# Optimization experiments

Hardware: AMD Instinct MI355X
Metric: run time of the kernel (lower is better)

The kernel has to match this reference:

```python
import jax, jax.numpy as jnp
import numpy as np

N = 500_000   # points
D = 256       # num_features
K = 512       # number of foreground instances
OUT = 32      # out_channels


def setup_inputs() -> dict:
    key = jax.random.key(0)
    k1, k2, k3, k4, k5, k6 = jax.random.split(key, 6)
    features = jax.random.normal(k1, (N, D), dtype=jnp.float32)
    coords = jax.random.normal(k2, (N, 3), dtype=jnp.float32)
    # ids in [-1, K), -1 = background (guaranteed present in expectation)
    instance_ids = jax.random.randint(k3, (N,), -1, K, dtype=jnp.int32)
    # MLP params (torch Linear weight [out,in] stored transposed as [in,out])
    W1 = jax.random.normal(k4, (D, 64), dtype=jnp.float32) * (1.0 / np.sqrt(D))
    W2 = jax.random.normal(k5, (64, 64), dtype=jnp.float32) * (1.0 / np.sqrt(64))
    W3 = jax.random.normal(k6, (64, OUT), dtype=jnp.float32) * (1.0 / np.sqrt(64))
    b3 = jnp.zeros((OUT,), dtype=jnp.float32)
    return {
        "features": features,
        "coords": coords,
        "instance_ids": instance_ids,
        "num_instances": K,
        "W1": W1,
        "W2": W2,
        "W3": W3,
        "b3": b3,
    }


def reference(features, coords, instance_ids, num_instances, W1, W2, W3, b3):
    # Background (-1) points are routed to an extra dummy segment and dropped.
    seg = jnp.where(instance_ids >= 0, instance_ids, num_instances)
    nseg = num_instances + 1

    ones = jnp.ones((features.shape[0],), dtype=features.dtype)
    counts = jax.ops.segment_sum(ones, seg, num_segments=nseg)[:num_instances]  # [K]
    denom = jnp.maximum(counts, 1.0)[:, None]

    feat_sum = jax.ops.segment_sum(features, seg, num_segments=nseg)[:num_instances]  # [K, D]
    embeddings = feat_sum / denom  # per-instance feature mean (== prototype.F.mean(0))

    coord_sum = jax.ops.segment_sum(coords, seg, num_segments=nseg)[:num_instances]  # [K, 3]
    centroids = coord_sum / denom  # scatter_mean of coordinates

    # tiny MLP: Linear(D,64,no bias) -> ReLU -> Linear(64,64,no bias) -> ReLU -> Linear(64,OUT,bias)
    h = jax.nn.relu(embeddings @ W1)
    h = jax.nn.relu(h @ W2)
    out = h @ W3 + b3  # [K, OUT]

    return embeddings, centroids, out
```

## Files before the change

### kernel.cpp

```cpp
#include <hip/hip_runtime.h>

#define DFEAT 256
#define KINST 512
#define OUTC  32
#define CHUNK 4096
#define BUCKET_CHUNK 2048

__global__ __launch_bounds__(256) void hist_kernel(const int* __restrict__ ids,
                                                   int* __restrict__ counts, int n) {
    __shared__ int hist[KINST];
    int start = blockIdx.x * CHUNK;
    int len = n - start;
    if (len > CHUNK) len = CHUNK;
    for (int b = threadIdx.x; b < KINST; b += 256) hist[b] = 0;
    __syncthreads();
    for (int l = threadIdx.x; l < len; l += 256) {
        int id = ids[start + l];
        if (id >= 0) atomicAdd(&hist[id], 1);
    }
    __syncthreads();
    for (int b = threadIdx.x; b < KINST; b += 256) {
        int c = hist[b];
        if (c) atomicAdd(&counts[b], c);
    }
}

__global__ void scan_kernel(const int* __restrict__ counts, int* __restrict__ offsets) {
    __shared__ int s[KINST];
    int t = threadIdx.x;
    int c = counts[t];
    s[t] = c;
    __syncthreads();
    for (int off = 1; off < KINST; off <<= 1) {
        int add = (t >= off) ? s[t - off] : 0;
        __syncthreads();
        s[t] += add;
        __syncthreads();
    }
    offsets[t] = s[t] - c;
}

__global__ __launch_bounds__(256) void scatter2_kernel(const int* __restrict__ ids,
                                                       const int* __restrict__ offsets,
                                                       int* __restrict__ cursor,
                                                       int* __restrict__ bucket, int n) {
    __shared__ int ids_s[CHUNK];
    __shared__ int hist[KINST];
    __shared__ int bases[KINST];
    __shared__ int lcur[KINST];
    int start = blockIdx.x * CHUNK;
    int len = n - start;
    if (len > CHUNK) len = CHUNK;
    for (int b = threadIdx.x; b < KINST; b += 256) { hist[b] = 0; lcur[b] = 0; }
    for (int l = threadIdx.x; l < len; l += 256) ids_s[l] = ids[start + l];
    __syncthreads();
    for (int l = threadIdx.x; l < len; l += 256) {
        int id = ids_s[l];
        if (id >= 0) atomicAdd(&hist[id], 1);
    }
    __syncthreads();
    for (int b = threadIdx.x; b < KINST; b += 256) {
        int c = hist[b];
        bases[b] = c ? (offsets[b] + atomicAdd(&cursor[b], c)) : 0;
    }
    __syncthreads();
    for (int l = threadIdx.x; l < len; l += 256) {
        int id = ids_s[l];
        if (id >= 0) {
            int w = atomicAdd(&lcur[id], 1);
            bucket[bases[id] + w] = start + l;
        }
    }
}

__global__ __launch_bounds__(512) void gather_kernel(const float4* __restrict__ feat4,
                                                     const float* __restrict__ coords,
                                                     const int* __restrict__ bucket,
                                                     const int* __restrict__ offsets,
                                                     const int* __restrict__ counts,
                                                     float* __restrict__ emb_out,
                                                     float* __restrict__ cent_out) {
    __shared__ int bl[BUCKET_CHUNK];
    __shared__ float red[2048];

    int k   = blockIdx.x;
    int off = offsets[k];
    int cnt = counts[k];

    int sub = threadIdx.x >> 6;
    int f4  = threadIdx.x & 63;

    float a0x = 0.f, a0y = 0.f, a0z = 0.f, a0w = 0.f;
    float a1x = 0.f, a1y = 0.f, a1z = 0.f, a1w = 0.f;
    float cx = 0.f, cy = 0.f, cz = 0.f;

    for (int base = 0; base < cnt; base += BUCKET_CHUNK) {
        int chunk = cnt - base;
        if (chunk > BUCKET_CHUNK) chunk = BUCKET_CHUNK;
        for (int t = threadIdx.x; t < chunk; t += 512) bl[t] = bucket[off + base + t];
        __syncthreads();

        for (int t = threadIdx.x; t < chunk; t += 512) {
            long r = bl[t];
            cx += coords[r * 3 + 0];
            cy += coords[r * 3 + 1];
            cz += coords[r * 3 + 2];
        }

        int i = sub;
        for (; i + 8 < chunk; i += 16) {
            int r0 = bl[i];
            int r1 = bl[i + 8];
            float4 v0 = feat4[(long)r0 * 64 + f4];
            float4 v1 = feat4[(long)r1 * 64 + f4];
            a0x += v0.x; a0y += v0.y; a0z += v0.z; a0w += v0.w;
            a1x += v1.x; a1y += v1.y; a1z += v1.z; a1w += v1.w;
        }
        if (i < chunk) {
            int r = bl[i];
            float4 v = feat4[(long)r * 64 + f4];
            a0x += v.x; a0y += v.y; a0z += v.z; a0w += v.w;
        }
        __syncthreads();
    }

    a0x += a1x; a0y += a1y; a0z += a1z; a0w += a1w;

    float inv = 1.0f / (float)(cnt > 1 ? cnt : 1);

    red[threadIdx.x * 4 + 0] = a0x;
    red[threadIdx.x * 4 + 1] = a0y;
    red[threadIdx.x * 4 + 2] = a0z;
    red[threadIdx.x * 4 + 3] = a0w;
    __syncthreads();
    if (sub == 0) {
        float tx = 0.f, ty = 0.f, tz = 0.f, tw = 0.f;
        #pragma unroll
        for (int s = 0; s < 8; s++) {
            int b = (s * 64 + f4) * 4;
            tx += red[b + 0]; ty += red[b + 1]; tz += red[b + 2]; tw += red[b + 3];
        }
        float4 o;
        o.x = tx * inv; o.y = ty * inv; o.z = tz * inv; o.w = tw * inv;
        ((float4*)emb_out)[(long)k * 64 + f4] = o;
    }
    __syncthreads();

    red[threadIdx.x]        = cx;
    red[512  + threadIdx.x] = cy;
    red[1024 + threadIdx.x] = cz;
    __syncthreads();
    for (int s = 256; s > 0; s >>= 1) {
        if (threadIdx.x < s) {
            red[threadIdx.x]        += red[threadIdx.x + s];
            red[512  + threadIdx.x] += red[512  + threadIdx.x + s];
            red[1024 + threadIdx.x] += red[1024 + threadIdx.x + s];
        }
        __syncthreads();
    }
    if (threadIdx.x == 0) {
        cent_out[k * 3 + 0] = red[0]    * inv;
        cent_out[k * 3 + 1] = red[512]  * inv;
        cent_out[k * 3 + 2] = red[1024] * inv;
    }
}

__global__ __launch_bounds__(64) void mlp_kernel(const float* __restrict__ emb,
                                                 const float* __restrict__ W1,
                                                 const float* __restrict__ W2,
                                                 const float* __restrict__ W3,
                                                 const float* __restrict__ b3,
                                                 float* __restrict__ mlp_out) {
    int k = blockIdx.x;
    int j = threadIdx.x;
    __shared__ float e[DFEAT];
    __shared__ float h1[64];
    __shared__ float h2[64];

    float4 ev = ((const float4*)emb)[(long)k * 64 + j];
    e[j * 4 + 0] = ev.x; e[j * 4 + 1] = ev.y; e[j * 4 + 2] = ev.z; e[j * 4 + 3] = ev.w;
    __syncthreads();

    float acc = 0.f;
    #pragma unroll 8
    for (int d = 0; d < DFEAT; d++) acc += e[d] * W1[d * 64 + j];
    h1[j] = fmaxf(acc, 0.f);
    __syncthreads();

    acc = 0.f;
    #pragma unroll 8
    for (int d = 0; d < 64; d++) acc += h1[d] * W2[d * 64 + j];
    h2[j] = fmaxf(acc, 0.f);
    __syncthreads();

    if (j < OUTC) {
        float o = b3[j];
        #pragma unroll 8
        for (int d = 0; d < 64; d++) o += h2[d] * W3[d * OUTC + j];
        mlp_out[k * OUTC + j] = o;
    }
}

extern "C" void kernel_launch(void* const* d_in, const int* in_sizes, int n_in,
                              void* d_out, int out_size, void* d_ws, size_t ws_size,
                              hipStream_t stream) {
    const float* features = (const float*)d_in[0];
    const float* coords   = (const float*)d_in[1];
    const int*   ids      = (const int*)d_in[2];
    const float* W1 = (const float*)d_in[4];
    const float* W2 = (const float*)d_in[5];
    const float* W3 = (const float*)d_in[6];
    const float* b3 = (const float*)d_in[7];

    int n = in_sizes[2];

    float* out      = (float*)d_out;
    float* emb_out  = out;
    float* cent_out = out + (long)KINST * DFEAT;
    float* mlp_out  = cent_out + (long)KINST * 3;

    char* ws = (char*)d_ws;
    int* counts  = (int*)(ws + 0);
    int* cursor  = (int*)(ws + 2048);
    int* offsets = (int*)(ws + 4096);
    int* bucket  = (int*)(ws + 6144);

    hipMemsetAsync(d_ws, 0, 4096, stream);

    int blocksHS = (n + CHUNK - 1) / CHUNK;
    hist_kernel<<<blocksHS, 256, 0, stream>>>(ids, counts, n);
    scan_kernel<<<1, KINST, 0, stream>>>(counts, offsets);
    scatter2_kernel<<<blocksHS, 256, 0, stream>>>(ids, offsets, cursor, bucket, n);
    gather_kernel<<<KINST, 512, 0, stream>>>((const float4*)features, coords, bucket,
                                             offsets, counts, emb_out, cent_out);
    mlp_kernel<<<KINST, 64, 0, stream>>>(emb_out, W1, W2, W3, b3, mlp_out);
}
```

Before: 711.9 us.

## Fuse centroid sums into histogram, precompute per-block bases, fuse MLP into gather

```diff
diff --git a/kernel.cpp b/kernel.cpp
--- a/kernel.cpp
+++ b/kernel.cpp
@@ -6,26 +6,51 @@
 #define CHUNK 4096
 #define BUCKET_CHUNK 2048
 
-__global__ __launch_bounds__(256) void hist_kernel(const int* __restrict__ ids,
-                                                   int* __restrict__ counts, int n) {
+__global__ __launch_bounds__(256) void hist_coords_kernel(
+        const int* __restrict__ ids, const float* __restrict__ coords,
+        int* __restrict__ counts, float* __restrict__ csum,
+        int* __restrict__ blockhist, int n) {
     __shared__ int hist[KINST];
+    __shared__ float sx[KINST], sy[KINST], sz[KINST];
     int start = blockIdx.x * CHUNK;
     int len = n - start;
     if (len > CHUNK) len = CHUNK;
-    for (int b = threadIdx.x; b < KINST; b += 256) hist[b] = 0;
+    for (int b = threadIdx.x; b < KINST; b += 256) {
+        hist[b] = 0; sx[b] = 0.f; sy[b] = 0.f; sz[b] = 0.f;
+    }
     __syncthreads();
     for (int l = threadIdx.x; l < len; l += 256) {
         int id = ids[start + l];
-        if (id >= 0) atomicAdd(&hist[id], 1);
+        if (id >= 0) {
+            long p = (long)(start + l) * 3;
+            float x = coords[p + 0];
+            float y = coords[p + 1];
+            float z = coords[p + 2];
+            atomicAdd(&hist[id], 1);
+            atomicAdd(&sx[id], x);
+            atomicAdd(&sy[id], y);
+            atomicAdd(&sz[id], z);
+        }
     }
     __syncthreads();
     for (int b = threadIdx.x; b < KINST; b += 256) {
         int c = hist[b];
-        if (c) atomicAdd(&counts[b], c);
-    }
-}
-
-__global__ void scan_kernel(const int* __restrict__ counts, int* __restrict__ offsets) {
+        blockhist[blockIdx.x * KINST + b] = c;
+        if (c) {
+            atomicAdd(&counts[b], c);
+            atomicAdd(&csum[b * 3 + 0], sx[b]);
+            atomicAdd(&csum[b * 3 + 1], sy[b]);
+            atomicAdd(&csum[b * 3 + 2], sz[b]);
+        }
+    }
+}
+
+__global__ void scan_kernel(const int* __restrict__ counts,
+                            const float* __restrict__ csum,
+                            int* __restrict__ offsets,
+                            const int* __restrict__ blockhist,
+                            int* __restrict__ blockbase,
+                            float* __restrict__ cent_out, int nblk) {
     __shared__ int s[KINST];
     int t = threadIdx.x;
     int c = counts[t];
@@ -37,35 +62,36 @@
         s[t] += add;
         __syncthreads();
     }
-    offsets[t] = s[t] - c;
-}
-
-__global__ __launch_bounds__(256) void scatter2_kernel(const int* __restrict__ ids,
-                                                       const int* __restrict__ offsets,
-                                                       int* __restrict__ cursor,
-                                                       int* __restrict__ bucket, int n) {
-    __shared__ int ids_s[CHUNK];
-    __shared__ int hist[KINST];
+    int excl = s[t] - c;
+    offsets[t] = excl;
+
+    float inv = 1.0f / (float)(c > 1 ? c : 1);
+    cent_out[t * 3 + 0] = csum[t * 3 + 0] * inv;
+    cent_out[t * 3 + 1] = csum[t * 3 + 1] * inv;
+    cent_out[t * 3 + 2] = csum[t * 3 + 2] * inv;
+
+    int base = excl;
+    for (int blk = 0; blk < nblk; ++blk) {
+        blockbase[blk * KINST + t] = base;
+        base += blockhist[blk * KINST + t];
+    }
+}
+
+__global__ __launch_bounds__(256) void scatter_kernel(
+        const int* __restrict__ ids, const int* __restrict__ blockbase,
+        int* __restrict__ bucket, int n) {
     __shared__ int bases[KINST];
     __shared__ int lcur[KINST];
     int start = blockIdx.x * CHUNK;
     int len = n - start;
     if (len > CHUNK) len = CHUNK;
-    for (int b = threadIdx.x; b < KINST; b += 256) { hist[b] = 0; lcur[b] = 0; }
-    for (int l = threadIdx.x; l < len; l += 256) ids_s[l] = ids[start + l];
+    for (int b = threadIdx.x; b < KINST; b += 256) {
+        bases[b] = blockbase[blockIdx.x * KINST + b];
+        lcur[b] = 0;
+    }
     __syncthreads();
     for (int l = threadIdx.x; l < len; l += 256) {
-        int id = ids_s[l];
-        if (id >= 0) atomicAdd(&hist[id], 1);
-    }
-    __syncthreads();
-    for (int b = threadIdx.x; b < KINST; b += 256) {
-        int c = hist[b];
-        bases[b] = c ? (offsets[b] + atomicAdd(&cursor[b], c)) : 0;
-    }
-    __syncthreads();
-    for (int l = threadIdx.x; l < len; l += 256) {
-        int id = ids_s[l];
+        int id = ids[start + l];
         if (id >= 0) {
             int w = atomicAdd(&lcur[id], 1);
             bucket[bases[id] + w] = start + l;
@@ -73,15 +99,19 @@
     }
 }
 
-__global__ __launch_bounds__(512) void gather_kernel(const float4* __restrict__ feat4,
-                                                     const float* __restrict__ coords,
-                                                     const int* __restrict__ bucket,
-                                                     const int* __restrict__ offsets,
-                                                     const int* __restrict__ counts,
-                                                     float* __restrict__ emb_out,
-                                                     float* __restrict__ cent_out) {
+__global__ __launch_bounds__(512) void gather_mlp_kernel(
+        const float4* __restrict__ feat4,
+        const int* __restrict__ bucket,
+        const int* __restrict__ offsets,
+        const int* __restrict__ counts,
+        const float* __restrict__ W1, const float* __restrict__ W2,
+        const float* __restrict__ W3, const float* __restrict__ b3,
+        float* __restrict__ emb_out, float* __restrict__ mlp_out) {
     __shared__ int bl[BUCKET_CHUNK];
     __shared__ float red[2048];
+    __shared__ float e[DFEAT];
+    __shared__ float h1[64];
+    __shared__ float h2[64];
 
     int k   = blockIdx.x;
     int off = offsets[k];
@@ -90,9 +120,10 @@
     int sub = threadIdx.x >> 6;
     int f4  = threadIdx.x & 63;
 
-    float a0x = 0.f, a0y = 0.f, a0z = 0.f, a0w = 0.f;
-    float a1x = 0.f, a1y = 0.f, a1z = 0.f, a1w = 0.f;
-    float cx = 0.f, cy = 0.f, cz = 0.f;
+    float a0x=0.f,a0y=0.f,a0z=0.f,a0w=0.f;
+    float a1x=0.f,a1y=0.f,a1z=0.f,a1w=0.f;
+    float a2x=0.f,a2y=0.f,a2z=0.f,a2w=0.f;
+    float a3x=0.f,a3y=0.f,a3z=0.f,a3w=0.f;
 
     for (int base = 0; base < cnt; base += BUCKET_CHUNK) {
         int chunk = cnt - base;
@@ -100,23 +131,22 @@
         for (int t = threadIdx.x; t < chunk; t += 512) bl[t] = bucket[off + base + t];
         __syncthreads();
 
-        for (int t = threadIdx.x; t < chunk; t += 512) {
-            long r = bl[t];
-            cx += coords[r * 3 + 0];
-            cy += coords[r * 3 + 1];
-            cz += coords[r * 3 + 2];
-        }
-
         int i = sub;
-        for (; i + 8 < chunk; i += 16) {
+        for (; i + 24 < chunk; i += 32) {
             int r0 = bl[i];
             int r1 = bl[i + 8];
+            int r2 = bl[i + 16];
+            int r3 = bl[i + 24];
             float4 v0 = feat4[(long)r0 * 64 + f4];
             float4 v1 = feat4[(long)r1 * 64 + f4];
+            float4 v2 = feat4[(long)r2 * 64 + f4];
+            float4 v3 = feat4[(long)r3 * 64 + f4];
             a0x += v0.x; a0y += v0.y; a0z += v0.z; a0w += v0.w;
             a1x += v1.x; a1y += v1.y; a1z += v1.z; a1w += v1.w;
-        }
-        if (i < chunk) {
+            a2x += v2.x; a2y += v2.y; a2z += v2.z; a2w += v2.w;
+            a3x += v3.x; a3y += v3.y; a3z += v3.z; a3w += v3.w;
+        }
+        for (; i < chunk; i += 8) {
             int r = bl[i];
             float4 v = feat4[(long)r * 64 + f4];
             a0x += v.x; a0y += v.y; a0z += v.z; a0w += v.w;
@@ -124,7 +154,10 @@
         __syncthreads();
     }
 
-    a0x += a1x; a0y += a1y; a0z += a1z; a0w += a1w;
+    a0x += a1x + a2x + a3x;
+    a0y += a1y + a2y + a3y;
+    a0z += a1z + a2z + a3z;
+    a0w += a1w + a2w + a3w;
 
     float inv = 1.0f / (float)(cnt > 1 ? cnt : 1);
 
@@ -143,56 +176,26 @@
         float4 o;
         o.x = tx * inv; o.y = ty * inv; o.z = tz * inv; o.w = tw * inv;
         ((float4*)emb_out)[(long)k * 64 + f4] = o;
-    }
-    __syncthreads();
-
-    red[threadIdx.x]        = cx;
-    red[512  + threadIdx.x] = cy;
-    red[1024 + threadIdx.x] = cz;
-    __syncthreads();
-    for (int s = 256; s > 0; s >>= 1) {
-        if (threadIdx.x < s) {
-            red[threadIdx.x]        += red[threadIdx.x + s];
-            red[512  + threadIdx.x] += red[512  + threadIdx.x + s];
-            red[1024 + threadIdx.x] += red[1024 + threadIdx.x + s];
-        }
-        __syncthreads();
-    }
-    if (threadIdx.x == 0) {
-        cent_out[k * 3 + 0] = red[0]    * inv;
-        cent_out[k * 3 + 1] = red[512]  * inv;
-        cent_out[k * 3 + 2] = red[1024] * inv;
-    }
-}
-
-__global__ __launch_bounds__(64) void mlp_kernel(const float* __restrict__ emb,
-                                                 const float* __restrict__ W1,
-                                                 const float* __restrict__ W2,
-                                                 const float* __restrict__ W3,
-                                                 const float* __restrict__ b3,
-                                                 float* __restrict__ mlp_out) {
-    int k = blockIdx.x;
+        e[f4 * 4 + 0] = o.x; e[f4 * 4 + 1] = o.y;
+        e[f4 * 4 + 2] = o.z; e[f4 * 4 + 3] = o.w;
+    }
+    __syncthreads();
+
     int j = threadIdx.x;
-    __shared__ float e[DFEAT];
-    __shared__ float h1[64];
-    __shared__ float h2[64];
-
-    float4 ev = ((const float4*)emb)[(long)k * 64 + j];
-    e[j * 4 + 0] = ev.x; e[j * 4 + 1] = ev.y; e[j * 4 + 2] = ev.z; e[j * 4 + 3] = ev.w;
-    __syncthreads();
-
-    float acc = 0.f;
-    #pragma unroll 8
-    for (int d = 0; d < DFEAT; d++) acc += e[d] * W1[d * 64 + j];
-    h1[j] = fmaxf(acc, 0.f);
-    __syncthreads();
-
-    acc = 0.f;
-    #pragma unroll 8
-    for (int d = 0; d < 64; d++) acc += h1[d] * W2[d * 64 + j];
-    h2[j] = fmaxf(acc, 0.f);
-    __syncthreads();
-
+    if (j < 64) {
+        float acc = 0.f;
+        #pragma unroll 8
+        for (int d = 0; d < DFEAT; d++) acc += e[d] * W1[d * 64 + j];
+        h1[j] = fmaxf(acc, 0.f);
+    }
+    __syncthreads();
+    if (j < 64) {
+        float acc = 0.f;
+        #pragma unroll 8
+        for (int d = 0; d < 64; d++) acc += h1[d] * W2[d * 64 + j];
+        h2[j] = fmaxf(acc, 0.f);
+    }
+    __syncthreads();
     if (j < OUTC) {
         float o = b3[j];
         #pragma unroll 8
@@ -213,6 +216,7 @@
     const float* b3 = (const float*)d_in[7];
 
     int n = in_sizes[2];
+    int nblk = (n + CHUNK - 1) / CHUNK;
 
     float* out      = (float*)d_out;
     float* emb_out  = out;
@@ -220,18 +224,22 @@
     float* mlp_out  = cent_out + (long)KINST * 3;
 
     char* ws = (char*)d_ws;
-    int* counts  = (int*)(ws + 0);
-    int* cursor  = (int*)(ws + 2048);
-    int* offsets = (int*)(ws + 4096);
-    int* bucket  = (int*)(ws + 6144);
-
-    hipMemsetAsync(d_ws, 0, 4096, stream);
-
-    int blocksHS = (n + CHUNK - 1) / CHUNK;
-    hist_kernel<<<blocksHS, 256, 0, stream>>>(ids, counts, n);
-    scan_kernel<<<1, KINST, 0, stream>>>(counts, offsets);
-    scatter2_kernel<<<blocksHS, 256, 0, stream>>>(ids, offsets, cursor, bucket, n);
-    gather_kernel<<<KINST, 512, 0, stream>>>((const float4*)features, coords, bucket,
-                                             offsets, counts, emb_out, cent_out);
-    mlp_kernel<<<KINST, 64, 0, stream>>>(emb_out, W1, W2, W3, b3, mlp_out);
-}
+    int*   counts    = (int*)(ws + 0);
+    float* csum      = (float*)(ws + 2048);
+    int*   offsets   = (int*)(ws + 8192);
+    int*   blockhist = (int*)(ws + 10240);
+    int*   blockbase = (int*)(ws + 10240 + (long)nblk * 2048);
+    int*   bucket    = (int*)(ws + 10240 + (long)nblk * 4096);
+
+    hipMemsetAsync(d_ws, 0, 8192, stream);
+
+    hist_coords_kernel<<<nblk, 256, 0, stream>>>(ids, coords, counts, csum,
+                                                 blockhist, n);
+    scan_kernel<<<1, KINST, 0, stream>>>(counts, csum, offsets, blockhist,
+                                         blockbase, cent_out, nblk);
+    scatter_kernel<<<nblk, 256, 0, stream>>>(ids, blockbase, bucket, n);
+    gather_mlp_kernel<<<KINST, 512, 0, stream>>>((const float4*)features, bucket,
+                                                 offsets, counts,
+                                                 W1, W2, W3, b3,
+                                                 emb_out, mlp_out);
+}
```

Result: slower. 730.9 us (+2.7%).
